# Kernel optimization log

Measured on AMD Instinct MI355X. Metric: run time of the kernel, lower is better.

The kernel has to match this reference:

```python
import jax, jax.numpy as jnp
import numpy as np

B, D, T, H, C = 256, 128, 512, 256, 10


def _xavier(key, shape):
    fan_in, fan_out = shape[0], shape[1]
    std = jnp.sqrt(2.0 / (fan_in + fan_out))
    return jax.random.normal(key, shape, dtype=jnp.float32) * std


def setup_inputs() -> dict:
    key = jax.random.key(0)
    ks = jax.random.split(key, 10)
    return {
        "x": jax.random.normal(ks[0], (B, D, T), dtype=jnp.float32),
        "W_gx": _xavier(ks[1], (D, H)),
        "W_ix": _xavier(ks[2], (D, H)),
        "W_fx": _xavier(ks[3], (D, H)),
        "W_ox": _xavier(ks[4], (D, H)),
        "W_gh": _xavier(ks[5], (H, H)),
        "W_ih": _xavier(ks[6], (H, H)),
        "W_fh": _xavier(ks[7], (H, H)),
        "W_oh": _xavier(ks[8], (H, H)),
        "b_g": jnp.zeros((H,), jnp.float32),
        "b_i": jnp.zeros((H,), jnp.float32),
        "b_f": jnp.zeros((H,), jnp.float32),
        "b_o": jnp.zeros((H,), jnp.float32),
        "W_ph": _xavier(ks[9], (H, C)),
        "b_p": jnp.zeros((C,), jnp.float32),
    }


def reference(x, W_gx, W_ix, W_fx, W_ox, W_gh, W_ih, W_fh, W_oh,
              b_g, b_i, b_f, b_o, W_ph, b_p):
    # x: [B, D, T] -> time-major [T, B, D]
    xs = jnp.transpose(x, (2, 0, 1))
    # Precompute all input-to-gate projections in one big GEMM per gate
    # (same math as per-step x_ @ W_*x, just batched over time).
    gx = jnp.einsum('tbd,dh->tbh', xs, W_gx) + b_g
    ix = jnp.einsum('tbd,dh->tbh', xs, W_ix) + b_i
    fx = jnp.einsum('tbd,dh->tbh', xs, W_fx) + b_f
    ox = jnp.einsum('tbd,dh->tbh', xs, W_ox) + b_o

    h0 = jnp.zeros((x.shape[0], W_gh.shape[0]), x.dtype)
    c0 = jnp.zeros_like(h0)

    def step(carry, inp):
        h, c = carry
        gx_t, ix_t, fx_t, ox_t = inp
        g = jnp.tanh(gx_t + h @ W_gh)
        i = jax.nn.sigmoid(ix_t + h @ W_ih)
        f = jax.nn.sigmoid(fx_t + h @ W_fh)
        o = jax.nn.sigmoid(ox_t + h @ W_oh)
        c = g * i + c * f
        h = jnp.tanh(c) * o
        return (h, c), None

    (h, c), _ = jax.lax.scan(step, (h0, c0), (gx, ix, fx, ox))
    return h @ W_ph + b_p
```

## Files before the change

kernel.cpp:

```cpp
#include <hip/hip_runtime.h>
#include <hip/hip_bf16.h>
#include <cstdint>

#define B_ 256
#define D_ 128
#define T_ 512
#define H_ 256
#define C_ 10

#define SENT 0xFFFFFFFFFFFFFFFFull

using f32x4 = __attribute__((ext_vector_type(4))) float;
using s16x8 = __attribute__((ext_vector_type(8))) short;

__device__ __forceinline__ unsigned short f2bf(float f) {
    union { float f; uint32_t u; } a; a.f = f;
    uint32_t u = a.u;
    uint32_t r = (u + 0x7fffu + ((u >> 16) & 1u)) >> 16;
    return (unsigned short)r;
}

__device__ __forceinline__ float sigm(float v) { return 1.0f / (1.0f + __expf(-v)); }

__global__ void xt_kernel(const float* __restrict__ x, unsigned short* __restrict__ xt) {
    __shared__ unsigned short tile[128][66];
    const int b  = blockIdx.x >> 3;
    const int t0 = (blockIdx.x & 7) << 6;
    const int tid = threadIdx.x;
    const int j  = tid & 63;
    const int dq = tid >> 6;

#pragma unroll
    for (int it = 0; it < 32; ++it) {
        int d = it * 4 + dq;
        tile[d][j] = f2bf(x[(size_t)(b * D_ + d) * T_ + t0 + j]);
    }
    __syncthreads();

    uint32_t* xt32 = (uint32_t*)xt;
#pragma unroll
    for (int it = 0; it < 16; ++it) {
        int tl = it * 4 + dq;
        int dp = j;
        uint32_t lo = tile[2 * dp][tl];
        uint32_t hi = tile[2 * dp + 1][tl];
        xt32[(size_t)((t0 + tl) * B_ + b) * (D_ / 2) + dp] = lo | (hi << 16);
    }
}

__global__ void __launch_bounds__(256) lstm_kernel(
    const float* __restrict__ Wgx, const float* __restrict__ Wix,
    const float* __restrict__ Wfx, const float* __restrict__ Wox,
    const float* __restrict__ Wgh, const float* __restrict__ Wih,
    const float* __restrict__ Wfh, const float* __restrict__ Woh,
    const float* __restrict__ bg,  const float* __restrict__ bi,
    const float* __restrict__ bf2, const float* __restrict__ bo,
    const unsigned short* __restrict__ xt,
    uint64_t* __restrict__ hbuf,
    float* __restrict__ hfin)
{
    __shared__ __align__(16) unsigned short Wh_s[4][16][264];
    __shared__ __align__(16) unsigned short Wx_s[4][16][136];
    __shared__ __align__(16) unsigned short h_s[16][264];
    __shared__ __align__(16) unsigned short x_s[16][136];
    __shared__ float pre_s[4][16][17];
    __shared__ float bias_s[4][16];

    const int tid  = threadIdx.x;
    const int bc   = blockIdx.x & 15;
    const int hc   = blockIdx.x >> 4;
    const int wave = tid >> 6;
    const int lane = tid & 63;
    const int mrow = lane & 15;
    const int quad = lane >> 4;

    const float* Wh[4] = {Wgh, Wih, Wfh, Woh};
    const float* Wx[4] = {Wgx, Wix, Wfx, Wox};
    const float* bias[4] = {bg, bi, bf2, bo};

#pragma unroll
    for (int g = 0; g < 4; ++g) {
        for (int it = 0; it < 16; ++it) {
            int idx = it * 256 + tid;
            int k = idx >> 4, c = idx & 15;
            Wh_s[g][c][k] = f2bf(Wh[g][(size_t)k * H_ + hc * 16 + c]);
        }
        for (int it = 0; it < 8; ++it) {
            int idx = it * 256 + tid;
            int k = idx >> 4, c = idx & 15;
            Wx_s[g][c][k] = f2bf(Wx[g][(size_t)k * H_ + hc * 16 + c]);
        }
    }
    if (tid < 64) bias_s[tid >> 4][tid & 15] = bias[tid >> 4][hc * 16 + (tid & 15)];
    __syncthreads();

    s16x8 wxf[4], whf[8];
#pragma unroll
    for (int kk = 0; kk < 4; ++kk)
        wxf[kk] = *(const s16x8*)&Wx_s[wave][mrow][kk * 32 + quad * 8];
#pragma unroll
    for (int kk = 0; kk < 8; ++kk)
        whf[kk] = *(const s16x8*)&Wh_s[wave][mrow][kk * 32 + quad * 8];

    const int b_l = tid >> 4;
    const int u_l = tid & 15;
    float c_st = 0.0f, h_st = 0.0f;

    uint64_t hv[4] = {SENT, SENT, SENT, SENT};

    uint4 xv = *(const uint4*)(xt + ((size_t)(0 * B_ + bc * 16 + b_l) * D_ + u_l * 8));

    for (int t = 0; t < T_; ++t) {
        *(uint4*)&x_s[b_l][u_l * 8] = xv;
        __syncthreads();

        if (t + 1 < T_)
            xv = *(const uint4*)(xt + ((size_t)((t + 1) * B_ + bc * 16 + b_l) * D_ + u_l * 8));

        f32x4 accx = {0.f, 0.f, 0.f, 0.f};
#pragma unroll
        for (int kk = 0; kk < 4; ++kk) {
            s16x8 a = *(const s16x8*)&x_s[mrow][kk * 32 + quad * 8];
            accx = __builtin_amdgcn_mfma_f32_16x16x32_bf16(a, wxf[kk], accx, 0, 0, 0);
        }

        if (t > 0) {
            const uint64_t* src = hbuf + (size_t)(t - 1) * (B_ * (H_ / 4));
            for (;;) {
                bool ok = true;
#pragma unroll
                for (int i = 0; i < 4; ++i) ok &= (hv[i] != SENT);
                if (ok) break;
                __builtin_amdgcn_s_sleep(1);
#pragma unroll
                for (int i = 0; i < 4; ++i)
                    if (hv[i] == SENT)
                        hv[i] = __hip_atomic_load(
                            &src[(size_t)(bc * 16 + i * 4 + wave) * (H_ / 4) + lane],
                            __ATOMIC_RELAXED, __HIP_MEMORY_SCOPE_AGENT);
            }
#pragma unroll
            for (int i = 0; i < 4; ++i)
                *(uint64_t*)&h_s[i * 4 + wave][lane * 4] = hv[i];
        }
        __syncthreads();

        f32x4 acc0 = {0.f, 0.f, 0.f, 0.f};
        f32x4 acc1 = {0.f, 0.f, 0.f, 0.f};
        if (t > 0) {
#pragma unroll
            for (int j = 0; j < 4; ++j) {
                s16x8 a  = *(const s16x8*)&h_s[mrow][(2 * j) * 32 + quad * 8];
                acc0 = __builtin_amdgcn_mfma_f32_16x16x32_bf16(a, whf[2 * j], acc0, 0, 0, 0);
                s16x8 a2 = *(const s16x8*)&h_s[mrow][(2 * j + 1) * 32 + quad * 8];
                acc1 = __builtin_amdgcn_mfma_f32_16x16x32_bf16(a2, whf[2 * j + 1], acc1, 0, 0, 0);
            }
        }

#pragma unroll
        for (int r = 0; r < 4; ++r)
            pre_s[wave][quad * 4 + r][mrow] = accx[r] + acc0[r] + acc1[r];
        __syncthreads();

        float pg = pre_s[0][b_l][u_l] + bias_s[0][u_l];
        float pi = pre_s[1][b_l][u_l] + bias_s[1][u_l];
        float pf = pre_s[2][b_l][u_l] + bias_s[2][u_l];
        float po = pre_s[3][b_l][u_l] + bias_s[3][u_l];
        float gg = 2.0f * sigm(2.0f * pg) - 1.0f;
        float ii = sigm(pi), ff = sigm(pf), oo = sigm(po);
        c_st = gg * ii + c_st * ff;
        float th = 2.0f * sigm(2.0f * c_st) - 1.0f;
        h_st = th * oo;

        uint32_t hb = f2bf(h_st);
        uint32_t p = hb | ((uint32_t)__shfl_down((int)hb, 1, 64) << 16);
        uint32_t q = (uint32_t)__shfl_down((int)p, 2, 64);
        if ((tid & 3) == 0) {
            uint64_t val = ((uint64_t)q << 32) | (uint64_t)p;
            uint64_t* dst = hbuf + (size_t)t * (B_ * (H_ / 4));
            __hip_atomic_store(&dst[(size_t)(bc * 16 + b_l) * (H_ / 4) + hc * 4 + (u_l >> 2)],
                               val, __ATOMIC_RELAXED, __HIP_MEMORY_SCOPE_AGENT);
        }

        if (t + 1 < T_) {
            const uint64_t* src = hbuf + (size_t)t * (B_ * (H_ / 4));
#pragma unroll
            for (int i = 0; i < 4; ++i)
                hv[i] = __hip_atomic_load(
                    &src[(size_t)(bc * 16 + i * 4 + wave) * (H_ / 4) + lane],
                    __ATOMIC_RELAXED, __HIP_MEMORY_SCOPE_AGENT);
        }
    }

    hfin[(size_t)(bc * 16 + b_l) * H_ + hc * 16 + u_l] = h_st;
}

__global__ void proj_kernel(const float* __restrict__ hfin, const float* __restrict__ Wph,
                            const float* __restrict__ bp, float* __restrict__ out) {
    int gid = blockIdx.x * 256 + threadIdx.x;
    if (gid >= B_ * C_) return;
    int b = gid / C_, cc = gid % C_;
    float acc = bp[cc];
#pragma unroll 8
    for (int u = 0; u < H_; ++u)
        acc += hfin[(size_t)b * H_ + u] * Wph[(size_t)u * C_ + cc];
    out[gid] = acc;
}

extern "C" void kernel_launch(void* const* d_in, const int* in_sizes, int n_in,
                              void* d_out, int out_size, void* d_ws, size_t ws_size,
                              hipStream_t stream) {
    const float* x   = (const float*)d_in[0];
    const float* Wgx = (const float*)d_in[1];
    const float* Wix = (const float*)d_in[2];
    const float* Wfx = (const float*)d_in[3];
    const float* Wox = (const float*)d_in[4];
    const float* Wgh = (const float*)d_in[5];
    const float* Wih = (const float*)d_in[6];
    const float* Wfh = (const float*)d_in[7];
    const float* Woh = (const float*)d_in[8];
    const float* bg  = (const float*)d_in[9];
    const float* bi  = (const float*)d_in[10];
    const float* bf2 = (const float*)d_in[11];
    const float* bo  = (const float*)d_in[12];
    const float* Wph = (const float*)d_in[13];
    const float* bp  = (const float*)d_in[14];

    const size_t hbuf_bytes = (size_t)T_ * B_ * (H_ / 4) * sizeof(uint64_t);

    char* ws = (char*)d_ws;
    uint64_t*       hbuf = (uint64_t*)ws;
    float*          hfin = (float*)(ws + hbuf_bytes);
    unsigned short* xt   = (unsigned short*)(ws + hbuf_bytes + (size_t)B_ * H_ * sizeof(float));

    hipMemsetAsync(hbuf, 0xFF, hbuf_bytes, stream);

    xt_kernel<<<B_ * (T_ / 64), 256, 0, stream>>>(x, xt);

    lstm_kernel<<<256, 256, 0, stream>>>(Wgx, Wix, Wfx, Wox, Wgh, Wih, Wfh, Woh,
                                         bg, bi, bf2, bo, xt, hbuf, hfin);

    proj_kernel<<<(B_ * C_ + 255) / 256, 256, 0, stream>>>(hfin, Wph, bp, (float*)d_out);
}
```

Measured before the change: 1.218 ms.

## Restructure persistent LSTM to 64 blocks with register-resident weights and no LDS

```diff
diff --git a/kernel.cpp b/kernel.cpp
--- a/kernel.cpp
+++ b/kernel.cpp
@@ -7,11 +7,11 @@
 #define T_ 512
 #define H_ 256
 #define C_ 10
-
-#define SENT 0xFFFFFFFFFFFFFFFFull
+#define S32 0xFFFFFFFFu
 
 using f32x4 = __attribute__((ext_vector_type(4))) float;
 using s16x8 = __attribute__((ext_vector_type(8))) short;
+using u32x4 = __attribute__((ext_vector_type(4))) unsigned int;
 
 __device__ __forceinline__ unsigned short f2bf(float f) {
     union { float f; uint32_t u; } a; a.f = f;
@@ -48,7 +48,20 @@
     }
 }
 
-__global__ void __launch_bounds__(256) lstm_kernel(
+#define ISSUE_H(base_)                                                                             \
+    do {                                                                                           \
+        const unsigned short* hsrc_ = (base_);                                                     \
+        asm volatile("global_load_dwordx4 %0, %1, off sc1"            : "=v"(hv[0]) : "v"(hsrc_)); \
+        asm volatile("global_load_dwordx4 %0, %1, off offset:64 sc1"  : "=v"(hv[1]) : "v"(hsrc_)); \
+        asm volatile("global_load_dwordx4 %0, %1, off offset:128 sc1" : "=v"(hv[2]) : "v"(hsrc_)); \
+        asm volatile("global_load_dwordx4 %0, %1, off offset:192 sc1" : "=v"(hv[3]) : "v"(hsrc_)); \
+        asm volatile("global_load_dwordx4 %0, %1, off offset:256 sc1" : "=v"(hv[4]) : "v"(hsrc_)); \
+        asm volatile("global_load_dwordx4 %0, %1, off offset:320 sc1" : "=v"(hv[5]) : "v"(hsrc_)); \
+        asm volatile("global_load_dwordx4 %0, %1, off offset:384 sc1" : "=v"(hv[6]) : "v"(hsrc_)); \
+        asm volatile("global_load_dwordx4 %0, %1, off offset:448 sc1" : "=v"(hv[7]) : "v"(hsrc_)); \
+    } while (0)
+
+__global__ void __launch_bounds__(256, 1) lstm_kernel(
     const float* __restrict__ Wgx, const float* __restrict__ Wix,
     const float* __restrict__ Wfx, const float* __restrict__ Wox,
     const float* __restrict__ Wgh, const float* __restrict__ Wih,
@@ -56,143 +69,125 @@
     const float* __restrict__ bg,  const float* __restrict__ bi,
     const float* __restrict__ bf2, const float* __restrict__ bo,
     const unsigned short* __restrict__ xt,
-    uint64_t* __restrict__ hbuf,
+    unsigned short* __restrict__ hbuf,
     float* __restrict__ hfin)
 {
-    __shared__ __align__(16) unsigned short Wh_s[4][16][264];
-    __shared__ __align__(16) unsigned short Wx_s[4][16][136];
-    __shared__ __align__(16) unsigned short h_s[16][264];
-    __shared__ __align__(16) unsigned short x_s[16][136];
-    __shared__ float pre_s[4][16][17];
-    __shared__ float bias_s[4][16];
-
     const int tid  = threadIdx.x;
-    const int bc   = blockIdx.x & 15;
-    const int hc   = blockIdx.x >> 4;
+    const int bc   = blockIdx.x >> 2;
+    const int hcq  = blockIdx.x & 3;
     const int wave = tid >> 6;
     const int lane = tid & 63;
     const int mrow = lane & 15;
     const int quad = lane >> 4;
-
-    const float* Wh[4] = {Wgh, Wih, Wfh, Woh};
-    const float* Wx[4] = {Wgx, Wix, Wfx, Wox};
-    const float* bias[4] = {bg, bi, bf2, bo};
-
+    const int u    = hcq * 64 + wave * 16 + mrow;
+
+    const float* WxA[4] = {Wgx, Wix, Wfx, Wox};
+    const float* WhA[4] = {Wgh, Wih, Wfh, Woh};
+
+    s16x8 wf[4][12];
 #pragma unroll
     for (int g = 0; g < 4; ++g) {
-        for (int it = 0; it < 16; ++it) {
-            int idx = it * 256 + tid;
-            int k = idx >> 4, c = idx & 15;
-            Wh_s[g][c][k] = f2bf(Wh[g][(size_t)k * H_ + hc * 16 + c]);
-        }
-        for (int it = 0; it < 8; ++it) {
-            int idx = it * 256 + tid;
-            int k = idx >> 4, c = idx & 15;
-            Wx_s[g][c][k] = f2bf(Wx[g][(size_t)k * H_ + hc * 16 + c]);
-        }
-    }
-    if (tid < 64) bias_s[tid >> 4][tid & 15] = bias[tid >> 4][hc * 16 + (tid & 15)];
-    __syncthreads();
-
-    s16x8 wxf[4], whf[8];
-#pragma unroll
-    for (int kk = 0; kk < 4; ++kk)
-        wxf[kk] = *(const s16x8*)&Wx_s[wave][mrow][kk * 32 + quad * 8];
-#pragma unroll
-    for (int kk = 0; kk < 8; ++kk)
-        whf[kk] = *(const s16x8*)&Wh_s[wave][mrow][kk * 32 + quad * 8];
-
-    const int b_l = tid >> 4;
-    const int u_l = tid & 15;
-    float c_st = 0.0f, h_st = 0.0f;
-
-    uint64_t hv[4] = {SENT, SENT, SENT, SENT};
-
-    uint4 xv = *(const uint4*)(xt + ((size_t)(0 * B_ + bc * 16 + b_l) * D_ + u_l * 8));
+#pragma unroll
+        for (int ks = 0; ks < 12; ++ks) {
+            const float* src = (ks < 4)
+                ? (WxA[g] + (size_t)(ks * 32 + quad * 8) * H_ + u)
+                : (WhA[g] + (size_t)((ks - 4) * 32 + quad * 8) * H_ + u);
+            s16x8 v;
+#pragma unroll
+            for (int j = 0; j < 8; ++j)
+                v[j] = (short)f2bf(src[(size_t)j * H_]);
+            wf[g][ks] = v;
+        }
+    }
+
+    const float bs0 = bg[u], bs1 = bi[u], bs2 = bf2[u], bs3 = bo[u];
+
+    float cst[4] = {0.f, 0.f, 0.f, 0.f};
+    float hst[4] = {0.f, 0.f, 0.f, 0.f};
+
+    u32x4 hv[8] = {};
+    u32x4 xa[4];
+
+    {
+        const unsigned short* p = xt + (size_t)(bc * 16 + mrow) * D_ + quad * 8;
+        xa[0] = *(const u32x4*)(p);      xa[1] = *(const u32x4*)(p + 32);
+        xa[2] = *(const u32x4*)(p + 64); xa[3] = *(const u32x4*)(p + 96);
+    }
 
     for (int t = 0; t < T_; ++t) {
-        *(uint4*)&x_s[b_l][u_l * 8] = xv;
-        __syncthreads();
+        f32x4 acc[4];
+#pragma unroll
+        for (int g = 0; g < 4; ++g) acc[g] = (f32x4){0.f, 0.f, 0.f, 0.f};
+
+#pragma unroll
+        for (int ks = 0; ks < 4; ++ks) {
+            s16x8 A = __builtin_bit_cast(s16x8, xa[ks]);
+#pragma unroll
+            for (int g = 0; g < 4; ++g)
+                acc[g] = __builtin_amdgcn_mfma_f32_16x16x32_bf16(A, wf[g][ks], acc[g], 0, 0, 0);
+        }
+        __builtin_amdgcn_sched_barrier(0);
+
+        if (t > 0) {
+            for (;;) {
+                asm volatile("s_waitcnt vmcnt(0)" ::: "memory");
+                __builtin_amdgcn_sched_barrier(0);
+                uint32_t m = 0;
+#pragma unroll
+                for (int i = 0; i < 8; ++i) {
+                    m = m > hv[i].x ? m : hv[i].x;
+                    m = m > hv[i].y ? m : hv[i].y;
+                    m = m > hv[i].z ? m : hv[i].z;
+                    m = m > hv[i].w ? m : hv[i].w;
+                }
+                if (__all(m != S32)) break;
+                __builtin_amdgcn_s_sleep(1);
+                ISSUE_H(hbuf + ((size_t)(t - 1) * B_ + bc * 16 + mrow) * H_ + quad * 8);
+            }
+#pragma unroll
+            for (int ks = 0; ks < 8; ++ks) {
+                s16x8 A = __builtin_bit_cast(s16x8, hv[ks]);
+#pragma unroll
+                for (int g = 0; g < 4; ++g)
+                    acc[g] = __builtin_amdgcn_mfma_f32_16x16x32_bf16(A, wf[g][4 + ks], acc[g], 0, 0, 0);
+            }
+        }
+
+        if (t + 1 < T_) {
+            const unsigned short* p = xt + ((size_t)(t + 1) * B_ + bc * 16 + mrow) * D_ + quad * 8;
+            xa[0] = *(const u32x4*)(p);      xa[1] = *(const u32x4*)(p + 32);
+            xa[2] = *(const u32x4*)(p + 64); xa[3] = *(const u32x4*)(p + 96);
+        }
+
+#pragma unroll
+        for (int r = 0; r < 4; ++r) {
+            float pg = acc[0][r] + bs0;
+            float pi = acc[1][r] + bs1;
+            float pf = acc[2][r] + bs2;
+            float po = acc[3][r] + bs3;
+            float gg = 2.0f * sigm(2.0f * pg) - 1.0f;
+            float ii = sigm(pi), ff = sigm(pf), oo = sigm(po);
+            cst[r] = gg * ii + cst[r] * ff;
+            hst[r] = (2.0f * sigm(2.0f * cst[r]) - 1.0f) * oo;
+        }
+
+        unsigned short* drow = hbuf + ((size_t)t * B_ + bc * 16 + quad * 4) * H_ + u;
+#pragma unroll
+        for (int r = 0; r < 4; ++r) {
+            uint32_t hb = f2bf(hst[r]);
+            uint32_t p2 = hb | ((uint32_t)__shfl_down((int)hb, 1, 64) << 16);
+            if ((mrow & 1) == 0)
+                __hip_atomic_store((uint32_t*)(drow + (size_t)r * H_), p2,
+                                   __ATOMIC_RELAXED, __HIP_MEMORY_SCOPE_AGENT);
+        }
 
         if (t + 1 < T_)
-            xv = *(const uint4*)(xt + ((size_t)((t + 1) * B_ + bc * 16 + b_l) * D_ + u_l * 8));
-
-        f32x4 accx = {0.f, 0.f, 0.f, 0.f};
-#pragma unroll
-        for (int kk = 0; kk < 4; ++kk) {
-            s16x8 a = *(const s16x8*)&x_s[mrow][kk * 32 + quad * 8];
-            accx = __builtin_amdgcn_mfma_f32_16x16x32_bf16(a, wxf[kk], accx, 0, 0, 0);
-        }
-
-        if (t > 0) {
-            const uint64_t* src = hbuf + (size_t)(t - 1) * (B_ * (H_ / 4));
-            for (;;) {
-                bool ok = true;
-#pragma unroll
-                for (int i = 0; i < 4; ++i) ok &= (hv[i] != SENT);
-                if (ok) break;
-                __builtin_amdgcn_s_sleep(1);
-#pragma unroll
-                for (int i = 0; i < 4; ++i)
-                    if (hv[i] == SENT)
-                        hv[i] = __hip_atomic_load(
-                            &src[(size_t)(bc * 16 + i * 4 + wave) * (H_ / 4) + lane],
-                            __ATOMIC_RELAXED, __HIP_MEMORY_SCOPE_AGENT);
-            }
-#pragma unroll
-            for (int i = 0; i < 4; ++i)
-                *(uint64_t*)&h_s[i * 4 + wave][lane * 4] = hv[i];
-        }
-        __syncthreads();
-
-        f32x4 acc0 = {0.f, 0.f, 0.f, 0.f};
-        f32x4 acc1 = {0.f, 0.f, 0.f, 0.f};
-        if (t > 0) {
-#pragma unroll
-            for (int j = 0; j < 4; ++j) {
-                s16x8 a  = *(const s16x8*)&h_s[mrow][(2 * j) * 32 + quad * 8];
-                acc0 = __builtin_amdgcn_mfma_f32_16x16x32_bf16(a, whf[2 * j], acc0, 0, 0, 0);
-                s16x8 a2 = *(const s16x8*)&h_s[mrow][(2 * j + 1) * 32 + quad * 8];
-                acc1 = __builtin_amdgcn_mfma_f32_16x16x32_bf16(a2, whf[2 * j + 1], acc1, 0, 0, 0);
-            }
-        }
-
-#pragma unroll
-        for (int r = 0; r < 4; ++r)
-            pre_s[wave][quad * 4 + r][mrow] = accx[r] + acc0[r] + acc1[r];
-        __syncthreads();
-
-        float pg = pre_s[0][b_l][u_l] + bias_s[0][u_l];
-        float pi = pre_s[1][b_l][u_l] + bias_s[1][u_l];
-        float pf = pre_s[2][b_l][u_l] + bias_s[2][u_l];
-        float po = pre_s[3][b_l][u_l] + bias_s[3][u_l];
-        float gg = 2.0f * sigm(2.0f * pg) - 1.0f;
-        float ii = sigm(pi), ff = sigm(pf), oo = sigm(po);
-        c_st = gg * ii + c_st * ff;
-        float th = 2.0f * sigm(2.0f * c_st) - 1.0f;
-        h_st = th * oo;
-
-        uint32_t hb = f2bf(h_st);
-        uint32_t p = hb | ((uint32_t)__shfl_down((int)hb, 1, 64) << 16);
-        uint32_t q = (uint32_t)__shfl_down((int)p, 2, 64);
-        if ((tid & 3) == 0) {
-            uint64_t val = ((uint64_t)q << 32) | (uint64_t)p;
-            uint64_t* dst = hbuf + (size_t)t * (B_ * (H_ / 4));
-            __hip_atomic_store(&dst[(size_t)(bc * 16 + b_l) * (H_ / 4) + hc * 4 + (u_l >> 2)],
-                               val, __ATOMIC_RELAXED, __HIP_MEMORY_SCOPE_AGENT);
-        }
-
-        if (t + 1 < T_) {
-            const uint64_t* src = hbuf + (size_t)t * (B_ * (H_ / 4));
-#pragma unroll
-            for (int i = 0; i < 4; ++i)
-                hv[i] = __hip_atomic_load(
-                    &src[(size_t)(bc * 16 + i * 4 + wave) * (H_ / 4) + lane],
-                    __ATOMIC_RELAXED, __HIP_MEMORY_SCOPE_AGENT);
-        }
-    }
-
-    hfin[(size_t)(bc * 16 + b_l) * H_ + hc * 16 + u_l] = h_st;
+            ISSUE_H(hbuf + ((size_t)t * B_ + bc * 16 + mrow) * H_ + quad * 8);
+    }
+
+#pragma unroll
+    for (int r = 0; r < 4; ++r)
+        hfin[(size_t)(bc * 16 + quad * 4 + r) * H_ + u] = hst[r];
 }
 
 __global__ void proj_kernel(const float* __restrict__ hfin, const float* __restrict__ Wph,
@@ -226,10 +221,10 @@
     const float* Wph = (const float*)d_in[13];
     const float* bp  = (const float*)d_in[14];
 
-    const size_t hbuf_bytes = (size_t)T_ * B_ * (H_ / 4) * sizeof(uint64_t);
+    const size_t hbuf_bytes = (size_t)T_ * B_ * H_ * 2;
 
     char* ws = (char*)d_ws;
-    uint64_t*       hbuf = (uint64_t*)ws;
+    unsigned short* hbuf = (unsigned short*)ws;
     float*          hfin = (float*)(ws + hbuf_bytes);
     unsigned short* xt   = (unsigned short*)(ws + hbuf_bytes + (size_t)B_ * H_ * sizeof(float));
 
@@ -237,8 +232,8 @@
 
     xt_kernel<<<B_ * (T_ / 64), 256, 0, stream>>>(x, xt);
 
-    lstm_kernel<<<256, 256, 0, stream>>>(Wgx, Wix, Wfx, Wox, Wgh, Wih, Wfh, Woh,
-                                         bg, bi, bf2, bo, xt, hbuf, hfin);
+    lstm_kernel<<<64, 256, 0, stream>>>(Wgx, Wix, Wfx, Wox, Wgh, Wih, Wfh, Woh,
+                                        bg, bi, bf2, bo, xt, hbuf, hfin);
 
     proj_kernel<<<(B_ * C_ + 255) / 256, 256, 0, stream>>>(hfin, Wph, bp, (float*)d_out);
 }
```

Measured after the change: 2.231 ms. +83.2%, slower.
